# Optimization experiments

Measured on AMD Instinct MI355X. Metric: run time of the kernel, lower is better.

The kernel has to match this reference:

```python
import jax, jax.numpy as jnp
import numpy as np

N, E, B = 50000, 800000, 64
IN, H, OUT = 64, 128, 64


def _gcn_norm(edge_index, num_nodes):
    # PyG gcn_norm with add_self_loops=True: A_hat = A + I, norm = d^-1/2[src]*d^-1/2[dst]
    loop = jnp.arange(num_nodes)
    src = jnp.concatenate([edge_index[0], loop])
    dst = jnp.concatenate([edge_index[1], loop])
    deg = jax.ops.segment_sum(jnp.ones_like(dst, dtype=jnp.float32), dst,
                              num_segments=num_nodes)  # >= 1 due to self-loops
    dis = deg ** -0.5
    norm = dis[src] * dis[dst]  # [E+N]
    return src, dst, norm


def _gcn_layer(x, W, b, src, dst, norm, num_nodes):
    h = x @ W                                   # linear first (GCNConv order)
    msg = h[src] * norm[:, None]                # gather + normalize, [E+N, H]
    out = jax.ops.segment_sum(msg, dst, num_segments=num_nodes)  # scatter-add
    return out + b


def setup_inputs() -> dict:
    key = jax.random.key(0)
    ks = jax.random.split(key, 12)
    x = jax.random.normal(ks[0], (N, IN), dtype=jnp.float32)
    edge_index = jax.random.randint(ks[1], (2, E), 0, N, dtype=jnp.int64)
    batch = jnp.sort(jax.random.randint(ks[2], (N,), 0, B, dtype=jnp.int64))

    def lin(k, fan_in, fan_out):
        s = 1.0 / np.sqrt(fan_in)
        return jax.random.uniform(k, (fan_in, fan_out), jnp.float32, -s, s)

    return {
        "x": x, "edge_index": edge_index, "batch": batch,
        "W1": lin(ks[3], IN, H), "b1": jnp.zeros((H,), jnp.float32),
        "W2": lin(ks[4], H, H),  "b2": jnp.zeros((H,), jnp.float32),
        "W3": lin(ks[5], H, H),  "b3": jnp.zeros((H,), jnp.float32),
        "W4": lin(ks[6], H, OUT), "b4": jnp.zeros((OUT,), jnp.float32),
    }


def reference(x, edge_index, batch, W1, b1, W2, b2, W3, b3, W4, b4):
    src, dst, norm = _gcn_norm(edge_index, N)
    h = jax.nn.relu(_gcn_layer(x, W1, b1, src, dst, norm, N))
    h = jax.nn.relu(_gcn_layer(h, W2, b2, src, dst, norm, N))
    # global mean pool over graphs
    sums = jax.ops.segment_sum(h, batch, num_segments=B)          # [B, H]
    cnts = jax.ops.segment_sum(jnp.ones((N,), jnp.float32), batch, num_segments=B)
    pooled = sums / jnp.maximum(cnts, 1.0)[:, None]
    # MLP head
    return jax.nn.relu(pooled @ W3 + b3) @ W4 + b4                # [B, OUT]
```

## Files before the change

### kernel.cpp

```cpp
#include <hip/hip_runtime.h>


__device__ __forceinline__ float ldf(const void* p, long long i, int f32) {
    if (f32) return ((const float*)p)[i];
    unsigned int u = ((const unsigned short*)p)[i];
    return __uint_as_float(u << 16);
}
__device__ __forceinline__ float bfl(unsigned int u) { return __uint_as_float(u << 16); }
__device__ __forceinline__ float bfh(unsigned int u) { return __uint_as_float(u & 0xFFFF0000u); }
__device__ __forceinline__ int ld_idx(const int* p, long long i, int i64) {
    return i64 ? p[2 * i] : p[i];
}
__device__ __forceinline__ unsigned short f2bf(float v) {
    unsigned int x = __float_as_uint(v);
    return (unsigned short)((x + 0x7FFFu + ((x >> 16) & 1u)) >> 16);
}
__device__ __forceinline__ int clampi(int v, int lo, int hi) {
    return v < lo ? lo : (v > hi ? hi : v);
}


__global__ void gnn_detect(const unsigned int* __restrict__ w1_words,
                           const int* __restrict__ ei_words,
                           int* __restrict__ flags) {
    __shared__ int cnt;
    __shared__ int orred;
    int t = threadIdx.x;
    if (t == 0) { cnt = 0; orred = 0; }
    __syncthreads();
    int c = 0, o = 0;
    for (int i = t; i < 512; i += 256) {
        unsigned int e = (w1_words[i] >> 7) & 0xFFu;
        if (e >= 100 && e <= 140) c++;
    }
    for (int i = t; i < 4096; i += 256) o |= ei_words[2 * i + 1];
    atomicAdd(&cnt, c);
    atomicOr(&orred, o);
    __syncthreads();
    if (t == 0) {
        flags[0] = (cnt > 256) ? 0 : 1;
        flags[1] = (orred == 0) ? 1 : 0;
    }
}

#define OW1 0
#define OB1 8192
#define OW2 8320
#define OB2 24704
#define OW3 24832
#define OB3 41216
#define OW4 41344
#define OB4 49536
#define OTOT 49600


__global__ void gnn_prep(const void* W1, const void* b1, const void* W2, const void* b2,
                         const void* W3, const void* b3, const void* W4, const void* b4,
                         const void* x, const int* __restrict__ flags,
                         int* __restrict__ degcnt, int* __restrict__ fillcnt,
                         float* __restrict__ pooled, float* __restrict__ cntf,
                         float* __restrict__ wsW, unsigned short* __restrict__ xb,
                         int N, int B) {
    const int f32 = flags[0];
    const int i = blockIdx.x * 256 + threadIdx.x;
    const int stride = gridDim.x * 256;
    for (int j = i; j < N; j += stride) { degcnt[j] = 0; fillcnt[j] = 0; }
    for (int j = i; j < B * 128; j += stride) pooled[j] = 0.f;
    for (int j = i; j < B; j += stride) cntf[j] = 0.f;
    for (int j = i; j < OTOT; j += stride) {
        float v;
        if      (j < OB1) v = ldf(W1, j - OW1, f32);
        else if (j < OW2) v = ldf(b1, j - OB1, f32);
        else if (j < OB2) v = ldf(W2, j - OW2, f32);
        else if (j < OW3) v = ldf(b2, j - OB2, f32);
        else if (j < OB3) v = ldf(W3, j - OW3, f32);
        else if (j < OW4) v = ldf(b3, j - OB3, f32);
        else if (j < OB4) v = ldf(W4, j - OW4, f32);
        else              v = ldf(b4, j - OB4, f32);
        wsW[j] = v;
    }
    if (f32) {
        const float* xf = (const float*)x;
        for (int j = i; j < N * 64; j += stride) xb[j] = f2bf(xf[j]);
    }
}


__global__ void gnn_hist(const int* __restrict__ ei, int E, int N,
                         const int* __restrict__ flags, int* __restrict__ degcnt) {
    int base = (blockIdx.x * 256 + threadIdx.x) * 4;
    if (base >= E) return;
    int i64 = flags[1];
    int m = min(4, E - base);
    int d[4];
#pragma unroll
    for (int j = 0; j < 4; ++j)
        if (j < m) d[j] = clampi(ld_idx(ei, (long long)E + base + j, i64), 0, N - 1);
#pragma unroll
    for (int j = 0; j < 4; ++j)
        if (j < m) atomicAdd(&degcnt[d[j]], 1);
}

__global__ void gnn_scan1(const int* __restrict__ cnt, int* __restrict__ excl,
                          int* __restrict__ sums, float* __restrict__ dis, int N) {
    __shared__ int sh[256];
    int t = threadIdx.x;
    int i = blockIdx.x * 256 + t;
    int v = (i < N) ? cnt[i] : 0;
    sh[t] = v;
    __syncthreads();
    for (int off = 1; off < 256; off <<= 1) {
        int a = (t >= off) ? sh[t - off] : 0;
        __syncthreads();
        sh[t] += a;
        __syncthreads();
    }
    if (i < N) {
        excl[i] = sh[t] - v;
        dis[i] = rsqrtf((float)v + 1.0f);
    }
    if (t == 255) sums[blockIdx.x] = sh[255];
}

__global__ void gnn_scan2(int* __restrict__ sums, int nb) {
    __shared__ int sh[256];
    int t = threadIdx.x;
    int v = (t < nb) ? sums[t] : 0;
    sh[t] = v;
    __syncthreads();
    for (int off = 1; off < 256; off <<= 1) {
        int a = (t >= off) ? sh[t - off] : 0;
        __syncthreads();
        sh[t] += a;
        __syncthreads();
    }
    if (t < nb) sums[t] = sh[t] - v;
}


template <bool SMALLN>
__global__ void gnn_fill(const int* __restrict__ ei, const int* __restrict__ excl,
                         const int* __restrict__ bsums, int* __restrict__ fillcnt,
                         void* __restrict__ csr, int E, int N,
                         const int* __restrict__ flags) {
    int e = blockIdx.x * 256 + threadIdx.x;
    if (e >= E) return;
    int i64 = flags[1];
    int s = clampi(ld_idx(ei, (long long)e, i64), 0, N - 1);
    int d = clampi(ld_idx(ei, (long long)E + e, i64), 0, N - 1);
    int rp = excl[d] + bsums[d >> 8];
    int pos = rp + atomicAdd(&fillcnt[d], 1);
    if (SMALLN) ((unsigned short*)csr)[pos] = (unsigned short)s;
    else        ((int*)csr)[pos] = s;
}

template <bool SMALLN>
__device__ __forceinline__ int csr_at(const void* csr, int e) {
    return SMALLN ? (int)((const unsigned short*)csr)[e] : ((const int*)csr)[e];
}


template <bool SMALLN>
__global__ __launch_bounds__(256) void gnn_agg_x(const void* __restrict__ x,
                                                 const unsigned short* __restrict__ xconv,
                                                 const int* __restrict__ excl,
                                                 const int* __restrict__ bsums,
                                                 const void* __restrict__ csr,
                                                 const float* __restrict__ dis,
                                                 const int* __restrict__ flags,
                                                 float* __restrict__ aggX, int N, int E) {
    const unsigned int* tab = flags[0] ? (const unsigned int*)xconv : (const unsigned int*)x;
    int t = threadIdx.x;
    int lane = t & 63;
    int n = blockIdx.x * 8 + (t >> 6) * 2 + (lane >> 5);
    if (n >= N) return;
    int fl = lane & 31;
    float dn = dis[n];
    float dn2 = dn * dn;
    unsigned int us = tab[(long long)n * 32 + fl];
    float a0 = bfl(us) * dn2, a1 = bfh(us) * dn2;
    int beg = excl[n] + bsums[n >> 8];
    int end = (n + 1 < N) ? (excl[n + 1] + bsums[(n + 1) >> 8]) : E;
    int e = beg;
    for (; e + 4 <= end; e += 4) {
        int s0 = csr_at<SMALLN>(csr, e),     s1 = csr_at<SMALLN>(csr, e + 1);
        int s2 = csr_at<SMALLN>(csr, e + 2), s3 = csr_at<SMALLN>(csr, e + 3);
        float w0 = dis[s0], w1 = dis[s1], w2 = dis[s2], w3 = dis[s3];
        unsigned int u0 = tab[(long long)s0 * 32 + fl];
        unsigned int u1 = tab[(long long)s1 * 32 + fl];
        unsigned int u2 = tab[(long long)s2 * 32 + fl];
        unsigned int u3 = tab[(long long)s3 * 32 + fl];
        w0 *= dn; w1 *= dn; w2 *= dn; w3 *= dn;
        a0 = fmaf(w0, bfl(u0), a0); a1 = fmaf(w0, bfh(u0), a1);
        a0 = fmaf(w1, bfl(u1), a0); a1 = fmaf(w1, bfh(u1), a1);
        a0 = fmaf(w2, bfl(u2), a0); a1 = fmaf(w2, bfh(u2), a1);
        a0 = fmaf(w3, bfl(u3), a0); a1 = fmaf(w3, bfh(u3), a1);
    }
    for (; e < end; ++e) {
        int s = csr_at<SMALLN>(csr, e);
        float w = dis[s] * dn;
        unsigned int u = tab[(long long)s * 32 + fl];
        a0 = fmaf(w, bfl(u), a0); a1 = fmaf(w, bfh(u), a1);
    }
    *(float2*)(aggX + (long long)n * 64 + fl * 2) = make_float2(a0, a1);
}


template <int K, bool RELU, bool OUTBF>
__global__ __launch_bounds__(256) void gnn_linear(const float* __restrict__ X,
                                                  const float* __restrict__ Wf,
                                                  const float* __restrict__ bias,
                                                  int N, void* __restrict__ out) {
    __shared__ float Wl[64 * 128];
    __shared__ float Xs[32 * K];
    const int t = threadIdx.x;
    const int nbase = blockIdx.x * 32;

#pragma unroll
    for (int it = 0; it < K / 32; ++it) {
        int i4 = t + it * 256;
        int n = nbase + (i4 * 4) / K;
        float4 v = make_float4(0.f, 0.f, 0.f, 0.f);
        if (n < N) v = ((const float4*)X)[(long long)nbase * (K / 4) + i4];
        ((float4*)Xs)[i4] = v;
    }

    const int fg = t & 31, ng = t >> 5;
    const int f0 = fg * 4, n0 = ng * 4;
    float4 acc[4];
#pragma unroll
    for (int j = 0; j < 4; ++j) acc[j] = make_float4(0.f, 0.f, 0.f, 0.f);

    for (int kc = 0; kc < K; kc += 64) {
        __syncthreads();
#pragma unroll
        for (int it = 0; it < 8; ++it) {
            int i4 = t + it * 256;
            ((float4*)Wl)[i4] = ((const float4*)(Wf + kc * 128))[i4];
        }
        __syncthreads();
#pragma unroll 4
        for (int k = 0; k < 64; ++k) {
            const float4 w = *(const float4*)&Wl[k * 128 + f0];
#pragma unroll
            for (int j = 0; j < 4; ++j) {
                float xv = Xs[(n0 + j) * K + kc + k];
                acc[j].x = fmaf(xv, w.x, acc[j].x);
                acc[j].y = fmaf(xv, w.y, acc[j].y);
                acc[j].z = fmaf(xv, w.z, acc[j].z);
                acc[j].w = fmaf(xv, w.w, acc[j].w);
            }
        }
    }

#pragma unroll
    for (int j = 0; j < 4; ++j) {
        int n = nbase + n0 + j;
        if (n >= N) continue;
        float4 a = acc[j];
        if (RELU) {
            const float4 b = *(const float4*)&bias[f0];
            a.x = fmaxf(a.x + b.x, 0.f);
            a.y = fmaxf(a.y + b.y, 0.f);
            a.z = fmaxf(a.z + b.z, 0.f);
            a.w = fmaxf(a.w + b.w, 0.f);
        }
        if (OUTBF) {
            uint2 u;
            u.x = (unsigned int)f2bf(a.x) | ((unsigned int)f2bf(a.y) << 16);
            u.y = (unsigned int)f2bf(a.z) | ((unsigned int)f2bf(a.w) << 16);
            *(uint2*)((unsigned short*)out + (long long)n * 128 + f0) = u;
        } else {
            *(float4*)((float*)out + (long long)n * 128 + f0) = a;
        }
    }
}


template <bool SMALLN>
__global__ __launch_bounds__(256) void gnn_agg_bf(const unsigned short* __restrict__ A2,
                                                  const int* __restrict__ excl,
                                                  const int* __restrict__ bsums,
                                                  const void* __restrict__ csr,
                                                  const float* __restrict__ dis,
                                                  const float* __restrict__ bias,
                                                  float* __restrict__ outC, int N, int E) {
    int t = threadIdx.x;
    int lane = t & 63;
    int n = blockIdx.x * 8 + (t >> 6) * 2 + (lane >> 5);
    if (n >= N) return;
    int fl = lane & 31;
    float dn = dis[n];
    float dn2 = dn * dn;
    uint2 us = *(const uint2*)(A2 + (long long)n * 128 + fl * 4);
    float a0 = bfl(us.x) * dn2, a1 = bfh(us.x) * dn2;
    float a2 = bfl(us.y) * dn2, a3 = bfh(us.y) * dn2;
    int beg = excl[n] + bsums[n >> 8];
    int end = (n + 1 < N) ? (excl[n + 1] + bsums[(n + 1) >> 8]) : E;
    int e = beg;
    for (; e + 4 <= end; e += 4) {
        int s0 = csr_at<SMALLN>(csr, e),     s1 = csr_at<SMALLN>(csr, e + 1);
        int s2 = csr_at<SMALLN>(csr, e + 2), s3 = csr_at<SMALLN>(csr, e + 3);
        float w0 = dis[s0], w1 = dis[s1], w2 = dis[s2], w3 = dis[s3];
        uint2 u0 = *(const uint2*)(A2 + (long long)s0 * 128 + fl * 4);
        uint2 u1 = *(const uint2*)(A2 + (long long)s1 * 128 + fl * 4);
        uint2 u2 = *(const uint2*)(A2 + (long long)s2 * 128 + fl * 4);
        uint2 u3 = *(const uint2*)(A2 + (long long)s3 * 128 + fl * 4);
        w0 *= dn; w1 *= dn; w2 *= dn; w3 *= dn;
        a0 = fmaf(w0, bfl(u0.x), a0); a1 = fmaf(w0, bfh(u0.x), a1);
        a2 = fmaf(w0, bfl(u0.y), a2); a3 = fmaf(w0, bfh(u0.y), a3);
        a0 = fmaf(w1, bfl(u1.x), a0); a1 = fmaf(w1, bfh(u1.x), a1);
        a2 = fmaf(w1, bfl(u1.y), a2); a3 = fmaf(w1, bfh(u1.y), a3);
        a0 = fmaf(w2, bfl(u2.x), a0); a1 = fmaf(w2, bfh(u2.x), a1);
        a2 = fmaf(w2, bfl(u2.y), a2); a3 = fmaf(w2, bfh(u2.y), a3);
        a0 = fmaf(w3, bfl(u3.x), a0); a1 = fmaf(w3, bfh(u3.x), a1);
        a2 = fmaf(w3, bfl(u3.y), a2); a3 = fmaf(w3, bfh(u3.y), a3);
    }
    for (; e < end; ++e) {
        int s = csr_at<SMALLN>(csr, e);
        float w = dis[s] * dn;
        uint2 u = *(const uint2*)(A2 + (long long)s * 128 + fl * 4);
        a0 = fmaf(w, bfl(u.x), a0); a1 = fmaf(w, bfh(u.x), a1);
        a2 = fmaf(w, bfl(u.y), a2); a3 = fmaf(w, bfh(u.y), a3);
    }
    const float4 b = *(const float4*)&bias[fl * 4];
    float4 o;
    o.x = fmaxf(a0 + b.x, 0.f);
    o.y = fmaxf(a1 + b.y, 0.f);
    o.z = fmaxf(a2 + b.z, 0.f);
    o.w = fmaxf(a3 + b.w, 0.f);
    *(float4*)(outC + (long long)n * 128 + fl * 4) = o;
}


#define PSTRIP 32
__global__ __launch_bounds__(128) void gnn_pool(const float* __restrict__ h,
                                                const int* __restrict__ batch,
                                                const int* __restrict__ flags,
                                                float* __restrict__ pooled,
                                                float* __restrict__ cntf, int N, int B) {
    int i64 = flags[1];
    int f = threadIdx.x;
    int n0 = blockIdx.x * PSTRIP;
    if (n0 >= N) return;
    int nend = min(n0 + PSTRIP, N);
    int cur = clampi(ld_idx(batch, n0, i64), 0, B - 1);
    float acc = 0.0f;
    float cc = 0.0f;
    for (int n = n0; n < nend; ++n) {
        int b = clampi(ld_idx(batch, n, i64), 0, B - 1);
        if (b != cur) {
            atomicAdd(&pooled[cur * 128 + f], acc);
            if (f == 0) atomicAdd(&cntf[cur], cc);
            acc = 0.0f; cc = 0.0f; cur = b;
        }
        acc += h[(long long)n * 128 + f];
        cc += 1.0f;
    }
    atomicAdd(&pooled[cur * 128 + f], acc);
    if (f == 0) atomicAdd(&cntf[cur], cc);
}


__global__ __launch_bounds__(128) void gnn_head(const float* __restrict__ pooled,
                                                const float* __restrict__ cntf,
                                                const float* __restrict__ W3,
                                                const float* __restrict__ b3,
                                                const float* __restrict__ W4,
                                                const float* __restrict__ b4,
                                                const int* __restrict__ flags,
                                                void* __restrict__ outv) {
    __shared__ float xs[128];
    __shared__ float rs[128];
    int b = blockIdx.x, f = threadIdx.x;
    float c = fmaxf(cntf[b], 1.0f);
    xs[f] = pooled[b * 128 + f] / c;
    __syncthreads();
    float acc = b3[f];
    for (int k = 0; k < 128; ++k) acc = fmaf(xs[k], W3[k * 128 + f], acc);
    rs[f] = fmaxf(acc, 0.f);
    __syncthreads();
    if (f < 64) {
        float a2 = b4[f];
        for (int k = 0; k < 128; ++k) a2 = fmaf(rs[k], W4[k * 64 + f], a2);
        if (flags[0]) ((float*)outv)[b * 64 + f] = a2;
        else          ((unsigned short*)outv)[b * 64 + f] = f2bf(a2);
    }
}


extern "C" void kernel_launch(void* const* d_in, const int* in_sizes, int n_in,
                              void* d_out, int out_size, void* d_ws, size_t ws_size,
                              hipStream_t stream) {
    const void* x  = d_in[0];
    const int* ei  = (const int*)d_in[1];
    const int* bat = (const int*)d_in[2];

    const int N = in_sizes[0] / 64;
    const int E = in_sizes[1] / 2;
    const int B = out_size / 64;
    const bool smalln = (N < 65536);

    char* p = (char*)d_ws;
    auto alloc = [&](size_t bytes) { void* q = (void*)p; p += (bytes + 255) & ~(size_t)255; return q; };
    int*   flags    = (int*)alloc(256);
    float* wsW      = (float*)alloc((size_t)OTOT * 4);
    int*   degcnt   = (int*)alloc((size_t)N * 4);
    int*   fillcnt  = (int*)alloc((size_t)N * 4);
    float* dis      = (float*)alloc((size_t)N * 4);
    int*   excl     = (int*)alloc((size_t)N * 4);
    int*   bsums    = (int*)alloc(1024);
    void*  csr      = alloc((size_t)E * (smalln ? 2 : 4));
    unsigned short* xb = (unsigned short*)alloc((size_t)N * 64 * 2);
    float* C2       = (float*)alloc((size_t)N * 128 * 4);
    float* H1       = (float*)alloc((size_t)N * 128 * 4);
    unsigned short* A2 = (unsigned short*)alloc((size_t)N * 128 * 2);
    float* pooled   = (float*)alloc((size_t)B * 128 * 4);
    float* cntf     = (float*)alloc((size_t)B * 4);
    (void)ws_size; (void)n_in;

    const int nbN = (N + 255) / 256;

    gnn_detect<<<1, 256, 0, stream>>>((const unsigned int*)d_in[3], ei, flags);
    gnn_prep<<<512, 256, 0, stream>>>(d_in[3], d_in[4], d_in[5], d_in[6],
                                      d_in[7], d_in[8], d_in[9], d_in[10],
                                      x, flags, degcnt, fillcnt, pooled, cntf,
                                      wsW, xb, N, B);

    gnn_hist<<<(E + 1023) / 1024, 256, 0, stream>>>(ei, E, N, flags, degcnt);
    gnn_scan1<<<nbN, 256, 0, stream>>>(degcnt, excl, bsums, dis, N);
    gnn_scan2<<<1, 256, 0, stream>>>(bsums, nbN);
    if (smalln)
        gnn_fill<true><<<(E + 255) / 256, 256, 0, stream>>>(ei, excl, bsums, fillcnt, csr, E, N, flags);
    else
        gnn_fill<false><<<(E + 255) / 256, 256, 0, stream>>>(ei, excl, bsums, fillcnt, csr, E, N, flags);

    const int nlin = (N + 31) / 32;
    const int nagg = (N + 7) / 8;

    if (smalln)
        gnn_agg_x<true><<<nagg, 256, 0, stream>>>(x, xb, excl, bsums, csr, dis, flags, C2, N, E);
    else
        gnn_agg_x<false><<<nagg, 256, 0, stream>>>(x, xb, excl, bsums, csr, dis, flags, C2, N, E);
    gnn_linear<64, true, false><<<nlin, 256, 0, stream>>>(C2, wsW + OW1, wsW + OB1, N, (void*)H1);

    gnn_linear<128, false, true><<<nlin, 256, 0, stream>>>(H1, wsW + OW2, wsW + OB2, N, (void*)A2);
    if (smalln)
        gnn_agg_bf<true><<<nagg, 256, 0, stream>>>(A2, excl, bsums, csr, dis, wsW + OB2, C2, N, E);
    else
        gnn_agg_bf<false><<<nagg, 256, 0, stream>>>(A2, excl, bsums, csr, dis, wsW + OB2, C2, N, E);

    gnn_pool<<<(N + PSTRIP - 1) / PSTRIP, 128, 0, stream>>>(C2, bat, flags, pooled, cntf, N, B);
    gnn_head<<<B, 128, 0, stream>>>(pooled, cntf, wsW + OW3, wsW + OB3,
                                    wsW + OW4, wsW + OB4, flags, d_out);
}
```

Before: 311.6 us.

## Fuse detect into prep, agg into linear1, pool into agg2; rank-based CSR fill

Folds format detection into the prep kernel, records atomic ranks in the histogram so the fill pass needs no second atomic counter, and fuses the layer-1 aggregation with its 64x128 linear+ReLU in one block. The layer-2 aggregation now atomically adds ReLU outputs straight into pooled sums, which removes the C2 round trip and the separate pool kernel. Per-graph counts are found by binary search in the head kernel, and the linear kernel reads weights directly from global memory instead of staging them in shared memory. This removes launches and intermediate traffic, at the cost of heavy atomic contention on only B*128 pooled addresses and an extra E-sized rank array.

```diff
diff --git a/kernel.cpp b/kernel.cpp
--- a/kernel.cpp
+++ b/kernel.cpp
@@ -17,30 +17,6 @@
 }
 __device__ __forceinline__ int clampi(int v, int lo, int hi) {
     return v < lo ? lo : (v > hi ? hi : v);
-}
-
-
-__global__ void gnn_detect(const unsigned int* __restrict__ w1_words,
-                           const int* __restrict__ ei_words,
-                           int* __restrict__ flags) {
-    __shared__ int cnt;
-    __shared__ int orred;
-    int t = threadIdx.x;
-    if (t == 0) { cnt = 0; orred = 0; }
-    __syncthreads();
-    int c = 0, o = 0;
-    for (int i = t; i < 512; i += 256) {
-        unsigned int e = (w1_words[i] >> 7) & 0xFFu;
-        if (e >= 100 && e <= 140) c++;
-    }
-    for (int i = t; i < 4096; i += 256) o |= ei_words[2 * i + 1];
-    atomicAdd(&cnt, c);
-    atomicOr(&orred, o);
-    __syncthreads();
-    if (t == 0) {
-        flags[0] = (cnt > 256) ? 0 : 1;
-        flags[1] = (orred == 0) ? 1 : 0;
-    }
 }
 
 #define OW1 0
@@ -56,17 +32,36 @@
 
 __global__ void gnn_prep(const void* W1, const void* b1, const void* W2, const void* b2,
                          const void* W3, const void* b3, const void* W4, const void* b4,
-                         const void* x, const int* __restrict__ flags,
-                         int* __restrict__ degcnt, int* __restrict__ fillcnt,
-                         float* __restrict__ pooled, float* __restrict__ cntf,
+                         const void* x, const int* __restrict__ ei,
+                         int* __restrict__ flags_out,
+                         int* __restrict__ degcnt, float* __restrict__ pooled,
                          float* __restrict__ wsW, unsigned short* __restrict__ xb,
                          int N, int B) {
-    const int f32 = flags[0];
-    const int i = blockIdx.x * 256 + threadIdx.x;
+    __shared__ int s_cnt, s_or;
+    const int t = threadIdx.x;
+    if (t == 0) { s_cnt = 0; s_or = 0; }
+    __syncthreads();
+    {
+        const unsigned int* w1w = (const unsigned int*)W1;
+        int c = 0, o = 0;
+        for (int i = t; i < 512; i += 256) {
+            unsigned int e = (w1w[i] >> 7) & 0xFFu;
+            if (e >= 100 && e <= 140) c++;
+        }
+        for (int i = t; i < 1024; i += 256) o |= ei[2 * i + 1];
+        atomicAdd(&s_cnt, c);
+        atomicOr(&s_or, o);
+    }
+    __syncthreads();
+    const int f32 = (s_cnt > 256) ? 0 : 1;
+    if (blockIdx.x == 0 && t == 0) {
+        flags_out[0] = f32;
+        flags_out[1] = (s_or == 0) ? 1 : 0;
+    }
+    const int i = blockIdx.x * 256 + t;
     const int stride = gridDim.x * 256;
-    for (int j = i; j < N; j += stride) { degcnt[j] = 0; fillcnt[j] = 0; }
+    for (int j = i; j < N; j += stride) degcnt[j] = 0;
     for (int j = i; j < B * 128; j += stride) pooled[j] = 0.f;
-    for (int j = i; j < B; j += stride) cntf[j] = 0.f;
     for (int j = i; j < OTOT; j += stride) {
         float v;
         if      (j < OB1) v = ldf(W1, j - OW1, f32);
@@ -87,18 +82,22 @@
 
 
 __global__ void gnn_hist(const int* __restrict__ ei, int E, int N,
-                         const int* __restrict__ flags, int* __restrict__ degcnt) {
+                         const int* __restrict__ flags, int* __restrict__ degcnt,
+                         int* __restrict__ rank) {
     int base = (blockIdx.x * 256 + threadIdx.x) * 4;
     if (base >= E) return;
     int i64 = flags[1];
     int m = min(4, E - base);
-    int d[4];
+    int d[4], r[4];
 #pragma unroll
     for (int j = 0; j < 4; ++j)
         if (j < m) d[j] = clampi(ld_idx(ei, (long long)E + base + j, i64), 0, N - 1);
 #pragma unroll
     for (int j = 0; j < 4; ++j)
-        if (j < m) atomicAdd(&degcnt[d[j]], 1);
+        if (j < m) r[j] = atomicAdd(&degcnt[d[j]], 1);
+#pragma unroll
+    for (int j = 0; j < 4; ++j)
+        if (j < m) rank[base + j] = r[j];
 }
 
 __global__ void gnn_scan1(const int* __restrict__ cnt, int* __restrict__ excl,
@@ -137,10 +136,9 @@
     if (t < nb) sums[t] = sh[t] - v;
 }
 
-
 template <bool SMALLN>
 __global__ void gnn_fill(const int* __restrict__ ei, const int* __restrict__ excl,
-                         const int* __restrict__ bsums, int* __restrict__ fillcnt,
+                         const int* __restrict__ bsums, const int* __restrict__ rank,
                          void* __restrict__ csr, int E, int N,
                          const int* __restrict__ flags) {
     int e = blockIdx.x * 256 + threadIdx.x;
@@ -148,8 +146,7 @@
     int i64 = flags[1];
     int s = clampi(ld_idx(ei, (long long)e, i64), 0, N - 1);
     int d = clampi(ld_idx(ei, (long long)E + e, i64), 0, N - 1);
-    int rp = excl[d] + bsums[d >> 8];
-    int pos = rp + atomicAdd(&fillcnt[d], 1);
+    int pos = excl[d] + bsums[d >> 8] + rank[e];
     if (SMALLN) ((unsigned short*)csr)[pos] = (unsigned short)s;
     else        ((int*)csr)[pos] = s;
 }
@@ -161,48 +158,90 @@
 
 
 template <bool SMALLN>
-__global__ __launch_bounds__(256) void gnn_agg_x(const void* __restrict__ x,
-                                                 const unsigned short* __restrict__ xconv,
-                                                 const int* __restrict__ excl,
-                                                 const int* __restrict__ bsums,
-                                                 const void* __restrict__ csr,
-                                                 const float* __restrict__ dis,
-                                                 const int* __restrict__ flags,
-                                                 float* __restrict__ aggX, int N, int E) {
+__global__ __launch_bounds__(256) void gnn_aggx_lin1(const void* __restrict__ x,
+                                                     const unsigned short* __restrict__ xconv,
+                                                     const int* __restrict__ excl,
+                                                     const int* __restrict__ bsums,
+                                                     const void* __restrict__ csr,
+                                                     const float* __restrict__ dis,
+                                                     const int* __restrict__ flags,
+                                                     const float* __restrict__ Wf,
+                                                     const float* __restrict__ bias,
+                                                     int N, int E, float* __restrict__ out) {
+    __shared__ float Xs[32 * 64];
     const unsigned int* tab = flags[0] ? (const unsigned int*)xconv : (const unsigned int*)x;
-    int t = threadIdx.x;
-    int lane = t & 63;
-    int n = blockIdx.x * 8 + (t >> 6) * 2 + (lane >> 5);
-    if (n >= N) return;
-    int fl = lane & 31;
-    float dn = dis[n];
-    float dn2 = dn * dn;
-    unsigned int us = tab[(long long)n * 32 + fl];
-    float a0 = bfl(us) * dn2, a1 = bfh(us) * dn2;
-    int beg = excl[n] + bsums[n >> 8];
-    int end = (n + 1 < N) ? (excl[n + 1] + bsums[(n + 1) >> 8]) : E;
-    int e = beg;
-    for (; e + 4 <= end; e += 4) {
-        int s0 = csr_at<SMALLN>(csr, e),     s1 = csr_at<SMALLN>(csr, e + 1);
-        int s2 = csr_at<SMALLN>(csr, e + 2), s3 = csr_at<SMALLN>(csr, e + 3);
-        float w0 = dis[s0], w1 = dis[s1], w2 = dis[s2], w3 = dis[s3];
-        unsigned int u0 = tab[(long long)s0 * 32 + fl];
-        unsigned int u1 = tab[(long long)s1 * 32 + fl];
-        unsigned int u2 = tab[(long long)s2 * 32 + fl];
-        unsigned int u3 = tab[(long long)s3 * 32 + fl];
-        w0 *= dn; w1 *= dn; w2 *= dn; w3 *= dn;
-        a0 = fmaf(w0, bfl(u0), a0); a1 = fmaf(w0, bfh(u0), a1);
-        a0 = fmaf(w1, bfl(u1), a0); a1 = fmaf(w1, bfh(u1), a1);
-        a0 = fmaf(w2, bfl(u2), a0); a1 = fmaf(w2, bfh(u2), a1);
-        a0 = fmaf(w3, bfl(u3), a0); a1 = fmaf(w3, bfh(u3), a1);
-    }
-    for (; e < end; ++e) {
-        int s = csr_at<SMALLN>(csr, e);
-        float w = dis[s] * dn;
-        unsigned int u = tab[(long long)s * 32 + fl];
-        a0 = fmaf(w, bfl(u), a0); a1 = fmaf(w, bfh(u), a1);
-    }
-    *(float2*)(aggX + (long long)n * 64 + fl * 2) = make_float2(a0, a1);
+    const int t = threadIdx.x;
+    const int nbase = blockIdx.x * 32;
+    const int lane = t & 63;
+    const int fl = lane & 31;
+
+#pragma unroll
+    for (int pass = 0; pass < 4; ++pass) {
+        int ln = pass * 8 + (t >> 6) * 2 + (lane >> 5);
+        int n = nbase + ln;
+        float a0 = 0.f, a1 = 0.f;
+        if (n < N) {
+            float dn = dis[n], dn2 = dn * dn;
+            unsigned int us = tab[(long long)n * 32 + fl];
+            a0 = bfl(us) * dn2; a1 = bfh(us) * dn2;
+            int beg = excl[n] + bsums[n >> 8];
+            int end = (n + 1 < N) ? (excl[n + 1] + bsums[(n + 1) >> 8]) : E;
+            int e = beg;
+            for (; e + 4 <= end; e += 4) {
+                int s0 = csr_at<SMALLN>(csr, e),     s1 = csr_at<SMALLN>(csr, e + 1);
+                int s2 = csr_at<SMALLN>(csr, e + 2), s3 = csr_at<SMALLN>(csr, e + 3);
+                float w0 = dis[s0], w1 = dis[s1], w2 = dis[s2], w3 = dis[s3];
+                unsigned int u0 = tab[(long long)s0 * 32 + fl];
+                unsigned int u1 = tab[(long long)s1 * 32 + fl];
+                unsigned int u2 = tab[(long long)s2 * 32 + fl];
+                unsigned int u3 = tab[(long long)s3 * 32 + fl];
+                w0 *= dn; w1 *= dn; w2 *= dn; w3 *= dn;
+                a0 = fmaf(w0, bfl(u0), a0); a1 = fmaf(w0, bfh(u0), a1);
+                a0 = fmaf(w1, bfl(u1), a0); a1 = fmaf(w1, bfh(u1), a1);
+                a0 = fmaf(w2, bfl(u2), a0); a1 = fmaf(w2, bfh(u2), a1);
+                a0 = fmaf(w3, bfl(u3), a0); a1 = fmaf(w3, bfh(u3), a1);
+            }
+            for (; e < end; ++e) {
+                int s = csr_at<SMALLN>(csr, e);
+                float w = dis[s] * dn;
+                unsigned int u = tab[(long long)s * 32 + fl];
+                a0 = fmaf(w, bfl(u), a0); a1 = fmaf(w, bfh(u), a1);
+            }
+        }
+        Xs[ln * 64 + fl * 2]     = a0;
+        Xs[ln * 64 + fl * 2 + 1] = a1;
+    }
+    __syncthreads();
+
+    const int fg = t & 31, ng = t >> 5;
+    const int f0 = fg * 4, n0 = ng * 4;
+    float4 acc[4];
+#pragma unroll
+    for (int j = 0; j < 4; ++j) acc[j] = make_float4(0.f, 0.f, 0.f, 0.f);
+#pragma unroll 8
+    for (int k = 0; k < 64; ++k) {
+        const float4 w = ((const float4*)(Wf + k * 128))[fg];
+#pragma unroll
+        for (int j = 0; j < 4; ++j) {
+            float xv = Xs[(n0 + j) * 64 + k];
+            acc[j].x = fmaf(xv, w.x, acc[j].x);
+            acc[j].y = fmaf(xv, w.y, acc[j].y);
+            acc[j].z = fmaf(xv, w.z, acc[j].z);
+            acc[j].w = fmaf(xv, w.w, acc[j].w);
+        }
+    }
+    const float4 b = *(const float4*)&bias[f0];
+#pragma unroll
+    for (int j = 0; j < 4; ++j) {
+        int n = nbase + n0 + j;
+        if (n >= N) continue;
+        float4 a = acc[j];
+        a.x = fmaxf(a.x + b.x, 0.f);
+        a.y = fmaxf(a.y + b.y, 0.f);
+        a.z = fmaxf(a.z + b.z, 0.f);
+        a.w = fmaxf(a.w + b.w, 0.f);
+        *(float4*)(out + (long long)n * 128 + f0) = a;
+    }
 }
 
 
@@ -211,7 +250,6 @@
                                                   const float* __restrict__ Wf,
                                                   const float* __restrict__ bias,
                                                   int N, void* __restrict__ out) {
-    __shared__ float Wl[64 * 128];
     __shared__ float Xs[32 * K];
     const int t = threadIdx.x;
     const int nbase = blockIdx.x * 32;
@@ -224,35 +262,25 @@
         if (n < N) v = ((const float4*)X)[(long long)nbase * (K / 4) + i4];
         ((float4*)Xs)[i4] = v;
     }
+    __syncthreads();
 
     const int fg = t & 31, ng = t >> 5;
     const int f0 = fg * 4, n0 = ng * 4;
     float4 acc[4];
 #pragma unroll
     for (int j = 0; j < 4; ++j) acc[j] = make_float4(0.f, 0.f, 0.f, 0.f);
-
-    for (int kc = 0; kc < K; kc += 64) {
-        __syncthreads();
-#pragma unroll
-        for (int it = 0; it < 8; ++it) {
-            int i4 = t + it * 256;
-            ((float4*)Wl)[i4] = ((const float4*)(Wf + kc * 128))[i4];
-        }
-        __syncthreads();
-#pragma unroll 4
-        for (int k = 0; k < 64; ++k) {
-            const float4 w = *(const float4*)&Wl[k * 128 + f0];
-#pragma unroll
-            for (int j = 0; j < 4; ++j) {
-                float xv = Xs[(n0 + j) * K + kc + k];
-                acc[j].x = fmaf(xv, w.x, acc[j].x);
-                acc[j].y = fmaf(xv, w.y, acc[j].y);
-                acc[j].z = fmaf(xv, w.z, acc[j].z);
-                acc[j].w = fmaf(xv, w.w, acc[j].w);
-            }
-        }
-    }
-
+#pragma unroll 8
+    for (int k = 0; k < K; ++k) {
+        const float4 w = ((const float4*)(Wf + k * 128))[fg];
+#pragma unroll
+        for (int j = 0; j < 4; ++j) {
+            float xv = Xs[(n0 + j) * K + k];
+            acc[j].x = fmaf(xv, w.x, acc[j].x);
+            acc[j].y = fmaf(xv, w.y, acc[j].y);
+            acc[j].z = fmaf(xv, w.z, acc[j].z);
+            acc[j].w = fmaf(xv, w.w, acc[j].w);
+        }
+    }
 #pragma unroll
     for (int j = 0; j < 4; ++j) {
         int n = nbase + n0 + j;
@@ -284,7 +312,10 @@
                                                   const void* __restrict__ csr,
                                                   const float* __restrict__ dis,
                                                   const float* __restrict__ bias,
-                                                  float* __restrict__ outC, int N, int E) {
+                                                  const int* __restrict__ batch,
+                                                  const int* __restrict__ flags,
+                                                  float* __restrict__ pooled,
+                                                  int N, int E, int B) {
     int t = threadIdx.x;
     int lane = t & 63;
     int n = blockIdx.x * 8 + (t >> 6) * 2 + (lane >> 5);
@@ -324,57 +355,42 @@
         a2 = fmaf(w, bfl(u.y), a2); a3 = fmaf(w, bfh(u.y), a3);
     }
     const float4 b = *(const float4*)&bias[fl * 4];
-    float4 o;
-    o.x = fmaxf(a0 + b.x, 0.f);
-    o.y = fmaxf(a1 + b.y, 0.f);
-    o.z = fmaxf(a2 + b.z, 0.f);
-    o.w = fmaxf(a3 + b.w, 0.f);
-    *(float4*)(outC + (long long)n * 128 + fl * 4) = o;
-}
-
-
-#define PSTRIP 32
-__global__ __launch_bounds__(128) void gnn_pool(const float* __restrict__ h,
+    a0 = fmaxf(a0 + b.x, 0.f);
+    a1 = fmaxf(a1 + b.y, 0.f);
+    a2 = fmaxf(a2 + b.z, 0.f);
+    a3 = fmaxf(a3 + b.w, 0.f);
+    int bg = clampi(ld_idx(batch, n, flags[1]), 0, B - 1);
+    float* pp = pooled + bg * 128 + fl * 4;
+    atomicAdd(pp + 0, a0);
+    atomicAdd(pp + 1, a1);
+    atomicAdd(pp + 2, a2);
+    atomicAdd(pp + 3, a3);
+}
+
+
+__global__ __launch_bounds__(128) void gnn_head(const float* __restrict__ pooled,
                                                 const int* __restrict__ batch,
-                                                const int* __restrict__ flags,
-                                                float* __restrict__ pooled,
-                                                float* __restrict__ cntf, int N, int B) {
-    int i64 = flags[1];
-    int f = threadIdx.x;
-    int n0 = blockIdx.x * PSTRIP;
-    if (n0 >= N) return;
-    int nend = min(n0 + PSTRIP, N);
-    int cur = clampi(ld_idx(batch, n0, i64), 0, B - 1);
-    float acc = 0.0f;
-    float cc = 0.0f;
-    for (int n = n0; n < nend; ++n) {
-        int b = clampi(ld_idx(batch, n, i64), 0, B - 1);
-        if (b != cur) {
-            atomicAdd(&pooled[cur * 128 + f], acc);
-            if (f == 0) atomicAdd(&cntf[cur], cc);
-            acc = 0.0f; cc = 0.0f; cur = b;
-        }
-        acc += h[(long long)n * 128 + f];
-        cc += 1.0f;
-    }
-    atomicAdd(&pooled[cur * 128 + f], acc);
-    if (f == 0) atomicAdd(&cntf[cur], cc);
-}
-
-
-__global__ __launch_bounds__(128) void gnn_head(const float* __restrict__ pooled,
-                                                const float* __restrict__ cntf,
                                                 const float* __restrict__ W3,
                                                 const float* __restrict__ b3,
                                                 const float* __restrict__ W4,
                                                 const float* __restrict__ b4,
                                                 const int* __restrict__ flags,
-                                                void* __restrict__ outv) {
+                                                void* __restrict__ outv, int N) {
     __shared__ float xs[128];
     __shared__ float rs[128];
+    __shared__ float cinv;
     int b = blockIdx.x, f = threadIdx.x;
-    float c = fmaxf(cntf[b], 1.0f);
-    xs[f] = pooled[b * 128 + f] / c;
+    if (f == 0) {
+        int i64 = flags[1];
+        int L = 0, R = N;
+        while (L < R) { int m = (L + R) >> 1; if (ld_idx(batch, m, i64) < b) L = m + 1; else R = m; }
+        int lo = L;
+        L = 0; R = N;
+        while (L < R) { int m = (L + R) >> 1; if (ld_idx(batch, m, i64) < b + 1) L = m + 1; else R = m; }
+        cinv = 1.0f / fmaxf((float)(L - lo), 1.0f);
+    }
+    __syncthreads();
+    xs[f] = pooled[b * 128 + f] * cinv;
     __syncthreads();
     float acc = b3[f];
     for (int k = 0; k < 128; ++k) acc = fmaf(xs[k], W3[k * 128 + f], acc);
@@ -406,51 +422,49 @@
     int*   flags    = (int*)alloc(256);
     float* wsW      = (float*)alloc((size_t)OTOT * 4);
     int*   degcnt   = (int*)alloc((size_t)N * 4);
-    int*   fillcnt  = (int*)alloc((size_t)N * 4);
     float* dis      = (float*)alloc((size_t)N * 4);
     int*   excl     = (int*)alloc((size_t)N * 4);
     int*   bsums    = (int*)alloc(1024);
+    int*   rank     = (int*)alloc((size_t)E * 4);
     void*  csr      = alloc((size_t)E * (smalln ? 2 : 4));
     unsigned short* xb = (unsigned short*)alloc((size_t)N * 64 * 2);
-    float* C2       = (float*)alloc((size_t)N * 128 * 4);
     float* H1       = (float*)alloc((size_t)N * 128 * 4);
     unsigned short* A2 = (unsigned short*)alloc((size_t)N * 128 * 2);
     float* pooled   = (float*)alloc((size_t)B * 128 * 4);
-    float* cntf     = (float*)alloc((size_t)B * 4);
     (void)ws_size; (void)n_in;
 
     const int nbN = (N + 255) / 256;
 
-    gnn_detect<<<1, 256, 0, stream>>>((const unsigned int*)d_in[3], ei, flags);
     gnn_prep<<<512, 256, 0, stream>>>(d_in[3], d_in[4], d_in[5], d_in[6],
                                       d_in[7], d_in[8], d_in[9], d_in[10],
-                                      x, flags, degcnt, fillcnt, pooled, cntf,
-                                      wsW, xb, N, B);
-
-    gnn_hist<<<(E + 1023) / 1024, 256, 0, stream>>>(ei, E, N, flags, degcnt);
+                                      x, ei, flags, degcnt, pooled, wsW, xb, N, B);
+
+    gnn_hist<<<(E + 1023) / 1024, 256, 0, stream>>>(ei, E, N, flags, degcnt, rank);
     gnn_scan1<<<nbN, 256, 0, stream>>>(degcnt, excl, bsums, dis, N);
     gnn_scan2<<<1, 256, 0, stream>>>(bsums, nbN);
     if (smalln)
-        gnn_fill<true><<<(E + 255) / 256, 256, 0, stream>>>(ei, excl, bsums, fillcnt, csr, E, N, flags);
+        gnn_fill<true><<<(E + 255) / 256, 256, 0, stream>>>(ei, excl, bsums, rank, csr, E, N, flags);
     else
-        gnn_fill<false><<<(E + 255) / 256, 256, 0, stream>>>(ei, excl, bsums, fillcnt, csr, E, N, flags);
+        gnn_fill<false><<<(E + 255) / 256, 256, 0, stream>>>(ei, excl, bsums, rank, csr, E, N, flags);
 
     const int nlin = (N + 31) / 32;
     const int nagg = (N + 7) / 8;
 
     if (smalln)
-        gnn_agg_x<true><<<nagg, 256, 0, stream>>>(x, xb, excl, bsums, csr, dis, flags, C2, N, E);
+        gnn_aggx_lin1<true><<<nlin, 256, 0, stream>>>(x, xb, excl, bsums, csr, dis, flags,
+                                                      wsW + OW1, wsW + OB1, N, E, H1);
     else
-        gnn_agg_x<false><<<nagg, 256, 0, stream>>>(x, xb, excl, bsums, csr, dis, flags, C2, N, E);
-    gnn_linear<64, true, false><<<nlin, 256, 0, stream>>>(C2, wsW + OW1, wsW + OB1, N, (void*)H1);
+        gnn_aggx_lin1<false><<<nlin, 256, 0, stream>>>(x, xb, excl, bsums, csr, dis, flags,
+                                                       wsW + OW1, wsW + OB1, N, E, H1);
 
     gnn_linear<128, false, true><<<nlin, 256, 0, stream>>>(H1, wsW + OW2, wsW + OB2, N, (void*)A2);
     if (smalln)
-        gnn_agg_bf<true><<<nagg, 256, 0, stream>>>(A2, excl, bsums, csr, dis, wsW + OB2, C2, N, E);
+        gnn_agg_bf<true><<<nagg, 256, 0, stream>>>(A2, excl, bsums, csr, dis, wsW + OB2,
+                                                   bat, flags, pooled, N, E, B);
     else
-        gnn_agg_bf<false><<<nagg, 256, 0, stream>>>(A2, excl, bsums, csr, dis, wsW + OB2, C2, N, E);
-
-    gnn_pool<<<(N + PSTRIP - 1) / PSTRIP, 128, 0, stream>>>(C2, bat, flags, pooled, cntf, N, B);
-    gnn_head<<<B, 128, 0, stream>>>(pooled, cntf, wsW + OW3, wsW + OB3,
-                                    wsW + OW4, wsW + OB4, flags, d_out);
-}
+        gnn_agg_bf<false><<<nagg, 256, 0, stream>>>(A2, excl, bsums, csr, dis, wsW + OB2,
+                                                    bat, flags, pooled, N, E, B);
+
+    gnn_head<<<B, 128, 0, stream>>>(pooled, bat, wsW + OW3, wsW + OB3,
+                                    wsW + OW4, wsW + OB4, flags, d_out, N);
+}
```

After: 528.7 us. +69.7%, slower.
